# Optimization experiments

Measured on AMD Instinct MI355X. Metric: run time of the kernel, lower is better.

## Reference

```python
import jax, jax.numpy as jnp
import numpy as np

N_NODES = 100000
N_EDGES = 1600000
D_IN, D_HID, D_OUT = 128, 64, 64


def setup_inputs() -> dict:
    key = jax.random.key(0)
    k0, k1, k2, k3 = jax.random.split(key, 4)
    X = jax.random.normal(k0, (N_NODES, D_IN), dtype=jnp.float32)
    E = jax.random.randint(k1, (2, N_EDGES), 0, N_NODES, dtype=jnp.int32)
    W1 = jax.random.normal(k2, (D_IN, D_HID), dtype=jnp.float32) * 0.05
    b1 = jnp.zeros((D_HID,), dtype=jnp.float32)
    W2 = jax.random.normal(k3, (D_HID, D_OUT), dtype=jnp.float32) * 0.05
    b2 = jnp.zeros((D_OUT,), dtype=jnp.float32)
    return {"V": N_NODES, "E": E, "X": X, "W1": W1, "b1": b1, "W2": W2, "b2": b2}


def _gcn_layer(X, W, b, src, dst, norm, n):
    # GCNConv: linear transform (no bias), gather, degree-normalize, scatter-add, + bias
    Xl = X @ W                              # [n, d_out]
    msg = Xl[src] * norm[:, None]           # [n_edges_sl, d_out] gather
    out = jax.ops.segment_sum(msg, dst, num_segments=n)  # scatter-add
    return out + b


def reference(V, E, X, W1, b1, W2, b2):
    n = X.shape[0]
    # add self loops (add_self_loops=True)
    loop = jnp.arange(n, dtype=E.dtype)
    src = jnp.concatenate([E[0], loop])
    dst = jnp.concatenate([E[1], loop])
    # symmetric gcn_norm: deg over target nodes (unit edge weights)
    deg = jax.ops.segment_sum(jnp.ones_like(dst, dtype=X.dtype), dst, num_segments=n)
    dinv = jnp.where(deg > 0, jax.lax.rsqrt(deg), 0.0)
    norm = dinv[src] * dinv[dst]
    H = jax.nn.relu(_gcn_layer(X, W1, b1, src, dst, norm, n))
    # last layer: no ReLU (matches torch module)
    return _gcn_layer(H, W2, b2, src, dst, norm, n)
```

## Files before the change

kernel.cpp:

```cpp
#include <hip/hip_runtime.h>

#define NT 256
#define TILE 256
#define TILE_SH 8
#define BSTRIDE 8192
#define BSTRIDE_SH 13
#define EPB 4096
#define ITB 16
#define NBUCK_PAD 512

static inline int cdiv(long long a, long long b) { return (int)((a + b - 1) / b); }

typedef unsigned int uint32;
typedef unsigned short ushort16;
typedef short bf16x8 __attribute__((ext_vector_type(8)));
typedef float f32x4 __attribute__((ext_vector_type(4)));

__device__ __forceinline__ ushort16 f2bf(float f) {
  uint32 u = __float_as_uint(f);
  u = (u + 0x7FFF + ((u >> 16) & 1)) >> 16;
  return (ushort16)u;
}
__device__ __forceinline__ float bflo(uint32 w) { return __uint_as_float(w << 16); }
__device__ __forceinline__ float bfhi(uint32 w) { return __uint_as_float(w & 0xFFFF0000u); }
__device__ __forceinline__ float bf2f(ushort16 h) { return __uint_as_float(((uint32)h) << 16); }

template <int K>
__device__ __forceinline__ void stage_W(const float* __restrict__ W,
                                        unsigned short* __restrict__ Wt) {
  constexpr int STR = K + 8;
  for (int i = threadIdx.x; i < K * 64; i += NT) {
    int k = i >> 6, nn = i & 63;
    Wt[nn * STR + k] = f2bf(W[i]);
  }
}

template <int K, int BFIN, int SPLIT>
__device__ __forceinline__ void gemm_tile(const void* __restrict__ Xp,
                                          const unsigned short* __restrict__ Wt,
                                          uint2* __restrict__ Yb, int n, int base) {
  constexpr int STR = K + 8;
  const int tid = threadIdx.x;
  const int w = tid >> 6;
  const int lane = tid & 63;
  const int r = lane & 15;
  const int quad = lane >> 4;
  const int rloc = w * 16 + r;
  const int v = base + rloc;

  f32x4 acc[4];
#pragma unroll
  for (int i = 0; i < 4; ++i) acc[i] = (f32x4)(0.f);

  if (BFIN) {
    const uint4* X4 = (const uint4*)Xp;
    bf16x8 xf[K / 32];
#pragma unroll
    for (int ks = 0; ks < K / 32; ++ks) {
      uint4 u = make_uint4(0u, 0u, 0u, 0u);
      if (v < n) u = X4[(size_t)v * (K / 8) + ks * 4 + quad];
      xf[ks] = *(const bf16x8*)&u;
    }
#pragma unroll
    for (int ks = 0; ks < K / 32; ++ks) {
      const int koff = ks * 32 + quad * 8;
#pragma unroll
      for (int nt = 0; nt < 4; ++nt) {
        bf16x8 wf = *(const bf16x8*)&Wt[(nt * 16 + r) * STR + koff];
        acc[nt] = __builtin_amdgcn_mfma_f32_16x16x32_bf16(wf, xf[ks], acc[nt], 0, 0, 0);
      }
    }
  } else {
    const float4* X4 = (const float4*)Xp;
    float4 a[K / 32][2];
#pragma unroll
    for (int ks = 0; ks < K / 32; ++ks) {
      a[ks][0] = make_float4(0.f, 0.f, 0.f, 0.f);
      a[ks][1] = make_float4(0.f, 0.f, 0.f, 0.f);
      if (v < n) {
        a[ks][0] = X4[(size_t)v * (K / 4) + ks * 8 + quad * 2];
        a[ks][1] = X4[(size_t)v * (K / 4) + ks * 8 + quad * 2 + 1];
      }
    }
#pragma unroll
    for (int ks = 0; ks < K / 32; ++ks) {
      float f[8] = {a[ks][0].x, a[ks][0].y, a[ks][0].z, a[ks][0].w,
                    a[ks][1].x, a[ks][1].y, a[ks][1].z, a[ks][1].w};
      bf16x8 xh, xl;
#pragma unroll
      for (int j = 0; j < 8; ++j) {
        ushort16 h = f2bf(f[j]);
        xh[j] = (short)h;
        if (SPLIT) xl[j] = (short)f2bf(f[j] - bf2f(h));
      }
      const int koff = ks * 32 + quad * 8;
#pragma unroll
      for (int nt = 0; nt < 4; ++nt) {
        bf16x8 wf = *(const bf16x8*)&Wt[(nt * 16 + r) * STR + koff];
        if (SPLIT)
          acc[nt] = __builtin_amdgcn_mfma_f32_16x16x32_bf16(wf, xl, acc[nt], 0, 0, 0);
        acc[nt] = __builtin_amdgcn_mfma_f32_16x16x32_bf16(wf, xh, acc[nt], 0, 0, 0);
      }
    }
  }

  if (v < n) {
#pragma unroll
    for (int nt = 0; nt < 4; ++nt) {
      uint2 u;
      u.x = (uint32)f2bf(acc[nt][0]) | ((uint32)f2bf(acc[nt][1]) << 16);
      u.y = (uint32)f2bf(acc[nt][2]) | ((uint32)f2bf(acc[nt][3]) << 16);
      Yb[(size_t)v * 16 + nt * 4 + quad] = u;
    }
  }
}

struct ScatSh {
  int cnt[NBUCK_PAD];
  int lcur[NBUCK_PAD];
  int delta[NBUCK_PAD];
  int hs[NT];
  uint32 sorted[EPB];
  unsigned short bid[EPB];
};
union FusedSh {
  unsigned short wt[64 * 136];
  ScatSh s;
};

__global__ __launch_bounds__(NT, 4) void k_fused(
    const int* __restrict__ src, const int* __restrict__ dst,
    int* __restrict__ bcursor, uint32* __restrict__ buck, int nE, int nbuck,
    int gscat, int ggemm, int ntile, const float* __restrict__ X,
    const float* __restrict__ W1, uint2* __restrict__ Yb, int n) {
  __shared__ FusedSh sm;
  if ((int)blockIdx.x >= gscat) {
    stage_W<128>(W1, sm.wt);
    __syncthreads();
    for (int tile = (int)blockIdx.x - gscat; tile < ntile; tile += ggemm)
      gemm_tile<128, 0, 1>(X, sm.wt, Yb, n, tile * 64);
    return;
  }
  const int t = threadIdx.x;
  for (int i = t; i < NBUCK_PAD; i += NT) sm.s.cnt[i] = 0;
  __syncthreads();
  const int e0 = blockIdx.x * EPB;
  const int ne = min(EPB, nE - e0);
  int dreg[ITB];
#pragma unroll
  for (int it = 0; it < ITB; ++it) {
    int e = e0 + it * NT + t;
    dreg[it] = (e < nE) ? dst[e] : -1;
    if (dreg[it] >= 0) atomicAdd(&sm.s.cnt[dreg[it] >> TILE_SH], 1);
  }
  __syncthreads();
  int c0 = sm.s.cnt[2 * t], c1 = sm.s.cnt[2 * t + 1];
  int ps = c0 + c1;
  sm.s.hs[t] = ps;
  __syncthreads();
  for (int o = 1; o < NT; o <<= 1) {
    int x = (t >= o) ? sm.s.hs[t - o] : 0;
    __syncthreads();
    sm.s.hs[t] += x;
    __syncthreads();
  }
  int lb0 = sm.s.hs[t] - ps;
  int lb1 = lb0 + c0;
  sm.s.lcur[2 * t] = lb0;
  sm.s.lcur[2 * t + 1] = lb1;
  {
    int b0 = 2 * t, b1 = 2 * t + 1;
    if (b0 < nbuck) {
      int g0 = c0 ? atomicAdd(&bcursor[b0], c0) : 0;
      sm.s.delta[b0] = (b0 << BSTRIDE_SH) + g0 - lb0;
    }
    if (b1 < nbuck) {
      int g1 = c1 ? atomicAdd(&bcursor[b1], c1) : 0;
      sm.s.delta[b1] = (b1 << BSTRIDE_SH) + g1 - lb1;
    }
  }
  __syncthreads();
#pragma unroll
  for (int it = 0; it < ITB; ++it) {
    int e = e0 + it * NT + t;
    if (dreg[it] >= 0) {
      int d = dreg[it];
      int b = d >> TILE_SH;
      int p = atomicAdd(&sm.s.lcur[b], 1);
      sm.s.sorted[p] = (uint32)src[e] | ((uint32)(d & (TILE - 1)) << 24);
      sm.s.bid[p] = (unsigned short)b;
    }
  }
  __syncthreads();
  for (int i = t; i < ne; i += NT) {
    int b = sm.s.bid[i];
    int g = sm.s.delta[b] + i;
    if (g < ((b + 1) << BSTRIDE_SH))
      buck[g] = sm.s.sorted[i];
  }
}

__global__ __launch_bounds__(NT) void k_bcsr(const uint32* __restrict__ buck,
                                             const int* __restrict__ bcursor,
                                             int2* __restrict__ rowspan,
                                             float* __restrict__ dinv,
                                             int* __restrict__ srcs, int n) {
  __shared__ int hist[TILE];
  __shared__ int hs[NT];
  __shared__ int off[TILE];
  __shared__ uint32 sarr[BSTRIDE];
  const int b = blockIdx.x;
  const int t = threadIdx.x;
  const int W = b * BSTRIDE;
  const int cntb = min(bcursor[b], BSTRIDE);
  const int v0 = b << TILE_SH;
  const int nv = min(TILE, n - v0);
  hist[t] = 0;
  __syncthreads();
  for (int i = t; i < cntb; i += NT) atomicAdd(&hist[buck[W + i] >> 24], 1);
  __syncthreads();
  int h = hist[t];
  hs[t] = h;
  __syncthreads();
  for (int o = 1; o < NT; o <<= 1) {
    int x = (t >= o) ? hs[t - o] : 0;
    __syncthreads();
    hs[t] += x;
    __syncthreads();
  }
  int ex = hs[t] - h;
  off[t] = ex;
  if (t < nv) {
    rowspan[v0 + t] = make_int2(W + ex, W + ex + h);
    dinv[v0 + t] = rsqrtf((float)(h + 1));
  }
  __syncthreads();
  for (int i = t; i < cntb; i += NT) {
    uint32 w = buck[W + i];
    int ld = (int)(w >> 24);
    int p = atomicAdd(&off[ld], 1);
    sarr[p] = w & 0x00FFFFFFu;
  }
  __syncthreads();
  for (int i = t; i < cntb; i += NT) srcs[W + i] = (int)sarr[i];
}

struct Acc8 {
  float a0, a1, a2, a3, a4, a5, a6, a7;
  __device__ __forceinline__ void madd(uint4 r, float s) {
    a0 = fmaf(bflo(r.x), s, a0); a1 = fmaf(bfhi(r.x), s, a1);
    a2 = fmaf(bflo(r.y), s, a2); a3 = fmaf(bfhi(r.y), s, a3);
    a4 = fmaf(bflo(r.z), s, a4); a5 = fmaf(bfhi(r.z), s, a5);
    a6 = fmaf(bflo(r.w), s, a6); a7 = fmaf(bfhi(r.w), s, a7);
  }
};

template <int RELU, int OUTBF>
__global__ __launch_bounds__(NT) void k_gather(const int2* __restrict__ rowspan,
                                               const int* __restrict__ srcs,
                                               const float* __restrict__ dinv,
                                               const uint4* __restrict__ Xn,
                                               const float* __restrict__ bias,
                                               void* __restrict__ outp, int n) {
  const int gt = blockIdx.x * NT + threadIdx.x;
  const int lane = threadIdx.x & 63;
  const int v = ((gt >> 6) << 1) + (lane >> 5);
  if (v >= n) return;
  const int l5 = lane & 31;
  const int part = l5 & 7;
  const int q = l5 >> 3;
  const int2 rs = rowspan[v];
  const int beg = rs.x, end = rs.y;
  const float dv = dinv[v];
  Acc8 A = {0.f, 0.f, 0.f, 0.f, 0.f, 0.f, 0.f, 0.f};
  int j = beg + q;
  for (; j + 4 < end; j += 8) {
    int s0 = srcs[j];
    int s1 = srcs[j + 4];
    float ds0 = dinv[s0];
    float ds1 = dinv[s1];
    uint4 r0 = Xn[(size_t)s0 * 8 + part];
    uint4 r1 = Xn[(size_t)s1 * 8 + part];
    A.madd(r0, ds0);
    A.madd(r1, ds1);
  }
  if (j < end) {
    int s = srcs[j];
    A.madd(Xn[(size_t)s * 8 + part], dinv[s]);
  }
#pragma unroll
  for (int m = 8; m <= 16; m <<= 1) {
    A.a0 += __shfl_xor(A.a0, m);
    A.a1 += __shfl_xor(A.a1, m);
    A.a2 += __shfl_xor(A.a2, m);
    A.a3 += __shfl_xor(A.a3, m);
    A.a4 += __shfl_xor(A.a4, m);
    A.a5 += __shfl_xor(A.a5, m);
    A.a6 += __shfl_xor(A.a6, m);
    A.a7 += __shfl_xor(A.a7, m);
  }
  if (q == 0) {
    uint4 wv = Xn[(size_t)v * 8 + part];
    const float4* b4 = (const float4*)bias;
    float4 b0 = b4[part * 2], b1 = b4[part * 2 + 1];
    float r0 = dv * (A.a0 + dv * bflo(wv.x)) + b0.x;
    float r1 = dv * (A.a1 + dv * bfhi(wv.x)) + b0.y;
    float r2 = dv * (A.a2 + dv * bflo(wv.y)) + b0.z;
    float r3 = dv * (A.a3 + dv * bfhi(wv.y)) + b0.w;
    float r4 = dv * (A.a4 + dv * bflo(wv.z)) + b1.x;
    float r5 = dv * (A.a5 + dv * bfhi(wv.z)) + b1.y;
    float r6 = dv * (A.a6 + dv * bflo(wv.w)) + b1.z;
    float r7 = dv * (A.a7 + dv * bfhi(wv.w)) + b1.w;
    if (RELU) {
      r0 = fmaxf(r0, 0.f); r1 = fmaxf(r1, 0.f); r2 = fmaxf(r2, 0.f); r3 = fmaxf(r3, 0.f);
      r4 = fmaxf(r4, 0.f); r5 = fmaxf(r5, 0.f); r6 = fmaxf(r6, 0.f); r7 = fmaxf(r7, 0.f);
    }
    if (OUTBF) {
      uint4 u;
      u.x = (uint32)f2bf(r0) | ((uint32)f2bf(r1) << 16);
      u.y = (uint32)f2bf(r2) | ((uint32)f2bf(r3) << 16);
      u.z = (uint32)f2bf(r4) | ((uint32)f2bf(r5) << 16);
      u.w = (uint32)f2bf(r6) | ((uint32)f2bf(r7) << 16);
      ((uint4*)outp)[(size_t)v * 8 + part] = u;
    } else {
      float4* o4 = (float4*)outp;
      o4[(size_t)v * 16 + part * 2] = make_float4(r0, r1, r2, r3);
      o4[(size_t)v * 16 + part * 2 + 1] = make_float4(r4, r5, r6, r7);
    }
  }
}

__global__ __launch_bounds__(NT, 4) void k_gemm2(const void* __restrict__ Xp,
                                                 const float* __restrict__ W,
                                                 uint2* __restrict__ Yb, int n,
                                                 int gg, int ntile) {
  __shared__ unsigned short Wt[64 * 72];
  stage_W<64>(W, Wt);
  __syncthreads();
  for (int tile = (int)blockIdx.x; tile < ntile; tile += gg)
    gemm_tile<64, 1, 0>(Xp, Wt, Yb, n, tile * 64);
}

extern "C" void kernel_launch(void* const* d_in, const int* in_sizes, int n_in,
                              void* d_out, int out_size, void* d_ws, size_t ws_size,
                              hipStream_t stream) {
  const int* E = (const int*)d_in[1];
  const float* X = (const float*)d_in[2];
  const float* W1 = (const float*)d_in[3];
  const float* b1 = (const float*)d_in[4];
  const float* W2 = (const float*)d_in[5];
  const float* b2 = (const float*)d_in[6];
  float* out = (float*)d_out;

  const int n = in_sizes[2] / 128;
  const int nE = in_sizes[1] / 2;
  const int* src = E;
  const int* dst = E + nE;
  const int nbuck = cdiv(n, TILE);

  char* ws = (char*)d_ws;
  size_t off = 0;
  auto alloc = [&](size_t bytes) {
    size_t o = off;
    off = (off + bytes + 255) & ~(size_t)255;
    return (void*)(ws + o);
  };
  int2* rowspan = (int2*)alloc((size_t)n * 8);
  float* dinv = (float*)alloc((size_t)n * 4);
  int* bcursor = (int*)alloc((size_t)nbuck * 4);
  uint32* buck = (uint32*)alloc((size_t)nbuck * BSTRIDE * 4);
  int* srcs = (int*)alloc((size_t)nbuck * BSTRIDE * 4);
  uint2* Xn = (uint2*)alloc((size_t)n * 64 * 2);
  uint2* H = (uint2*)alloc((size_t)n * 64 * 2);

  const int gscat = cdiv(nE, EPB);
  const int ntile = cdiv(n, 64);
  const int ggemm = 1024 - gscat;
  const int gthreads_blocks = cdiv((long long)n * 32, NT);

  hipMemsetAsync(bcursor, 0, (size_t)nbuck * 4, stream);

  k_fused<<<gscat + ggemm, NT, 0, stream>>>(src, dst, bcursor, buck, nE, nbuck,
                                            gscat, ggemm, ntile, X, W1, Xn, n);
  k_bcsr<<<nbuck, NT, 0, stream>>>(buck, bcursor, rowspan, dinv, srcs, n);

  k_gather<1, 1><<<gthreads_blocks, NT, 0, stream>>>(rowspan, srcs, dinv,
                                                     (const uint4*)Xn, b1, H, n);

  k_gemm2<<<1024, NT, 0, stream>>>(H, W2, Xn, n, 1024, ntile);
  k_gather<0, 0><<<gthreads_blocks, NT, 0, stream>>>(rowspan, srcs, dinv,
                                                     (const uint4*)Xn, b2, out, n);
}
```

Baseline: 233.1 us.

## Fuse layer-2 GEMM into layer-1 gather and add dynamic tile scheduling

```diff
diff --git a/kernel.cpp b/kernel.cpp
--- a/kernel.cpp
+++ b/kernel.cpp
@@ -35,7 +35,7 @@
   }
 }
 
-template <int K, int BFIN, int SPLIT>
+template <int K, int SPLIT>
 __device__ __forceinline__ void gemm_tile(const void* __restrict__ Xp,
                                           const unsigned short* __restrict__ Wt,
                                           uint2* __restrict__ Yb, int n, int base) {
@@ -52,55 +52,35 @@
 #pragma unroll
   for (int i = 0; i < 4; ++i) acc[i] = (f32x4)(0.f);
 
-  if (BFIN) {
-    const uint4* X4 = (const uint4*)Xp;
-    bf16x8 xf[K / 32];
-#pragma unroll
-    for (int ks = 0; ks < K / 32; ++ks) {
-      uint4 u = make_uint4(0u, 0u, 0u, 0u);
-      if (v < n) u = X4[(size_t)v * (K / 8) + ks * 4 + quad];
-      xf[ks] = *(const bf16x8*)&u;
-    }
-#pragma unroll
-    for (int ks = 0; ks < K / 32; ++ks) {
-      const int koff = ks * 32 + quad * 8;
-#pragma unroll
-      for (int nt = 0; nt < 4; ++nt) {
-        bf16x8 wf = *(const bf16x8*)&Wt[(nt * 16 + r) * STR + koff];
-        acc[nt] = __builtin_amdgcn_mfma_f32_16x16x32_bf16(wf, xf[ks], acc[nt], 0, 0, 0);
-      }
-    }
-  } else {
-    const float4* X4 = (const float4*)Xp;
-    float4 a[K / 32][2];
-#pragma unroll
-    for (int ks = 0; ks < K / 32; ++ks) {
-      a[ks][0] = make_float4(0.f, 0.f, 0.f, 0.f);
-      a[ks][1] = make_float4(0.f, 0.f, 0.f, 0.f);
-      if (v < n) {
-        a[ks][0] = X4[(size_t)v * (K / 4) + ks * 8 + quad * 2];
-        a[ks][1] = X4[(size_t)v * (K / 4) + ks * 8 + quad * 2 + 1];
-      }
-    }
-#pragma unroll
-    for (int ks = 0; ks < K / 32; ++ks) {
-      float f[8] = {a[ks][0].x, a[ks][0].y, a[ks][0].z, a[ks][0].w,
-                    a[ks][1].x, a[ks][1].y, a[ks][1].z, a[ks][1].w};
-      bf16x8 xh, xl;
-#pragma unroll
-      for (int j = 0; j < 8; ++j) {
-        ushort16 h = f2bf(f[j]);
-        xh[j] = (short)h;
-        if (SPLIT) xl[j] = (short)f2bf(f[j] - bf2f(h));
-      }
-      const int koff = ks * 32 + quad * 8;
-#pragma unroll
-      for (int nt = 0; nt < 4; ++nt) {
-        bf16x8 wf = *(const bf16x8*)&Wt[(nt * 16 + r) * STR + koff];
-        if (SPLIT)
-          acc[nt] = __builtin_amdgcn_mfma_f32_16x16x32_bf16(wf, xl, acc[nt], 0, 0, 0);
-        acc[nt] = __builtin_amdgcn_mfma_f32_16x16x32_bf16(wf, xh, acc[nt], 0, 0, 0);
-      }
+  const float4* X4 = (const float4*)Xp;
+  float4 a[K / 32][2];
+#pragma unroll
+  for (int ks = 0; ks < K / 32; ++ks) {
+    a[ks][0] = make_float4(0.f, 0.f, 0.f, 0.f);
+    a[ks][1] = make_float4(0.f, 0.f, 0.f, 0.f);
+    if (v < n) {
+      a[ks][0] = X4[(size_t)v * (K / 4) + ks * 8 + quad * 2];
+      a[ks][1] = X4[(size_t)v * (K / 4) + ks * 8 + quad * 2 + 1];
+    }
+  }
+#pragma unroll
+  for (int ks = 0; ks < K / 32; ++ks) {
+    float f[8] = {a[ks][0].x, a[ks][0].y, a[ks][0].z, a[ks][0].w,
+                  a[ks][1].x, a[ks][1].y, a[ks][1].z, a[ks][1].w};
+    bf16x8 xh, xl;
+#pragma unroll
+    for (int j = 0; j < 8; ++j) {
+      ushort16 h = f2bf(f[j]);
+      xh[j] = (short)h;
+      if (SPLIT) xl[j] = (short)f2bf(f[j] - bf2f(h));
+    }
+    const int koff = ks * 32 + quad * 8;
+#pragma unroll
+    for (int nt = 0; nt < 4; ++nt) {
+      bf16x8 wf = *(const bf16x8*)&Wt[(nt * 16 + r) * STR + koff];
+      if (SPLIT)
+        acc[nt] = __builtin_amdgcn_mfma_f32_16x16x32_bf16(wf, xl, acc[nt], 0, 0, 0);
+      acc[nt] = __builtin_amdgcn_mfma_f32_16x16x32_bf16(wf, xh, acc[nt], 0, 0, 0);
     }
   }
 
@@ -130,73 +110,81 @@
 
 __global__ __launch_bounds__(NT, 4) void k_fused(
     const int* __restrict__ src, const int* __restrict__ dst,
-    int* __restrict__ bcursor, uint32* __restrict__ buck, int nE, int nbuck,
-    int gscat, int ggemm, int ntile, const float* __restrict__ X,
-    const float* __restrict__ W1, uint2* __restrict__ Yb, int n) {
+    int* __restrict__ bcursor, int* __restrict__ tileCtr,
+    uint32* __restrict__ buck, int nE, int nbuck, int gscat, int ntile,
+    const float* __restrict__ X, const float* __restrict__ W1,
+    uint2* __restrict__ Yb, int n) {
   __shared__ FusedSh sm;
-  if ((int)blockIdx.x >= gscat) {
-    stage_W<128>(W1, sm.wt);
-    __syncthreads();
-    for (int tile = (int)blockIdx.x - gscat; tile < ntile; tile += ggemm)
-      gemm_tile<128, 0, 1>(X, sm.wt, Yb, n, tile * 64);
-    return;
-  }
+  __shared__ int stile;
   const int t = threadIdx.x;
-  for (int i = t; i < NBUCK_PAD; i += NT) sm.s.cnt[i] = 0;
-  __syncthreads();
-  const int e0 = blockIdx.x * EPB;
-  const int ne = min(EPB, nE - e0);
-  int dreg[ITB];
-#pragma unroll
-  for (int it = 0; it < ITB; ++it) {
-    int e = e0 + it * NT + t;
-    dreg[it] = (e < nE) ? dst[e] : -1;
-    if (dreg[it] >= 0) atomicAdd(&sm.s.cnt[dreg[it] >> TILE_SH], 1);
-  }
-  __syncthreads();
-  int c0 = sm.s.cnt[2 * t], c1 = sm.s.cnt[2 * t + 1];
-  int ps = c0 + c1;
-  sm.s.hs[t] = ps;
-  __syncthreads();
-  for (int o = 1; o < NT; o <<= 1) {
-    int x = (t >= o) ? sm.s.hs[t - o] : 0;
-    __syncthreads();
-    sm.s.hs[t] += x;
-    __syncthreads();
-  }
-  int lb0 = sm.s.hs[t] - ps;
-  int lb1 = lb0 + c0;
-  sm.s.lcur[2 * t] = lb0;
-  sm.s.lcur[2 * t + 1] = lb1;
-  {
-    int b0 = 2 * t, b1 = 2 * t + 1;
-    if (b0 < nbuck) {
-      int g0 = c0 ? atomicAdd(&bcursor[b0], c0) : 0;
-      sm.s.delta[b0] = (b0 << BSTRIDE_SH) + g0 - lb0;
-    }
-    if (b1 < nbuck) {
-      int g1 = c1 ? atomicAdd(&bcursor[b1], c1) : 0;
-      sm.s.delta[b1] = (b1 << BSTRIDE_SH) + g1 - lb1;
-    }
-  }
-  __syncthreads();
-#pragma unroll
-  for (int it = 0; it < ITB; ++it) {
-    int e = e0 + it * NT + t;
-    if (dreg[it] >= 0) {
-      int d = dreg[it];
-      int b = d >> TILE_SH;
-      int p = atomicAdd(&sm.s.lcur[b], 1);
-      sm.s.sorted[p] = (uint32)src[e] | ((uint32)(d & (TILE - 1)) << 24);
-      sm.s.bid[p] = (unsigned short)b;
-    }
-  }
-  __syncthreads();
-  for (int i = t; i < ne; i += NT) {
-    int b = sm.s.bid[i];
-    int g = sm.s.delta[b] + i;
-    if (g < ((b + 1) << BSTRIDE_SH))
-      buck[g] = sm.s.sorted[i];
+  if ((int)blockIdx.x < gscat) {
+    for (int i = t; i < NBUCK_PAD; i += NT) sm.s.cnt[i] = 0;
+    __syncthreads();
+    const int e0 = blockIdx.x * EPB;
+    const int ne = min(EPB, nE - e0);
+    int dreg[ITB];
+#pragma unroll
+    for (int it = 0; it < ITB; ++it) {
+      int e = e0 + it * NT + t;
+      dreg[it] = (e < nE) ? dst[e] : -1;
+      if (dreg[it] >= 0) atomicAdd(&sm.s.cnt[dreg[it] >> TILE_SH], 1);
+    }
+    __syncthreads();
+    int c0 = sm.s.cnt[2 * t], c1 = sm.s.cnt[2 * t + 1];
+    int ps = c0 + c1;
+    sm.s.hs[t] = ps;
+    __syncthreads();
+    for (int o = 1; o < NT; o <<= 1) {
+      int x = (t >= o) ? sm.s.hs[t - o] : 0;
+      __syncthreads();
+      sm.s.hs[t] += x;
+      __syncthreads();
+    }
+    int lb0 = sm.s.hs[t] - ps;
+    int lb1 = lb0 + c0;
+    sm.s.lcur[2 * t] = lb0;
+    sm.s.lcur[2 * t + 1] = lb1;
+    {
+      int b0 = 2 * t, b1 = 2 * t + 1;
+      if (b0 < nbuck) {
+        int g0 = c0 ? atomicAdd(&bcursor[b0], c0) : 0;
+        sm.s.delta[b0] = (b0 << BSTRIDE_SH) + g0 - lb0;
+      }
+      if (b1 < nbuck) {
+        int g1 = c1 ? atomicAdd(&bcursor[b1], c1) : 0;
+        sm.s.delta[b1] = (b1 << BSTRIDE_SH) + g1 - lb1;
+      }
+    }
+    __syncthreads();
+#pragma unroll
+    for (int it = 0; it < ITB; ++it) {
+      int e = e0 + it * NT + t;
+      if (dreg[it] >= 0) {
+        int d = dreg[it];
+        int b = d >> TILE_SH;
+        int p = atomicAdd(&sm.s.lcur[b], 1);
+        sm.s.sorted[p] = (uint32)src[e] | ((uint32)(d & (TILE - 1)) << 24);
+        sm.s.bid[p] = (unsigned short)b;
+      }
+    }
+    __syncthreads();
+    for (int i = t; i < ne; i += NT) {
+      int b = sm.s.bid[i];
+      int g = sm.s.delta[b] + i;
+      if (g < ((b + 1) << BSTRIDE_SH))
+        buck[g] = sm.s.sorted[i];
+    }
+    __syncthreads();
+  }
+  stage_W<128>(W1, sm.wt);
+  __syncthreads();
+  for (;;) {
+    if (t == 0) stile = atomicAdd(tileCtr, 1);
+    __syncthreads();
+    int tile = stile;
+    __syncthreads();
+    if (tile >= ntile) break;
+    gemm_tile<128, 1>(X, sm.wt, Yb, n, tile * 64);
   }
 }
 
@@ -255,13 +243,89 @@
   }
 };
 
-template <int RELU, int OUTBF>
-__global__ __launch_bounds__(NT) void k_gather(const int2* __restrict__ rowspan,
-                                               const int* __restrict__ srcs,
-                                               const float* __restrict__ dinv,
-                                               const uint4* __restrict__ Xn,
-                                               const float* __restrict__ bias,
-                                               void* __restrict__ outp, int n) {
+__global__ __launch_bounds__(NT) void k_gather_l1(
+    const int2* __restrict__ rowspan, const int* __restrict__ srcs,
+    const float* __restrict__ dinv, const uint4* __restrict__ Y1,
+    const float* __restrict__ bias, const float* __restrict__ W2,
+    uint32* __restrict__ Y2, int n) {
+  __shared__ float W2s[64 * 64];
+  __shared__ float hrow[8][72];
+  for (int i = threadIdx.x; i < 64 * 64; i += NT) W2s[i] = W2[i];
+
+  const int tid = threadIdx.x;
+  const int lane = tid & 63;
+  const int l5 = lane & 31;
+  const int part = l5 & 7;
+  const int q = l5 >> 3;
+  const int slot = ((tid >> 6) << 1) + (lane >> 5);
+  const int v = blockIdx.x * 8 + slot;
+  const bool act = v < n;
+
+  int2 rs = act ? rowspan[v] : make_int2(0, 0);
+  const int beg = rs.x, end = rs.y;
+  const float dv = act ? dinv[v] : 0.f;
+  Acc8 A = {0.f, 0.f, 0.f, 0.f, 0.f, 0.f, 0.f, 0.f};
+  int j = beg + q;
+  for (; j + 4 < end; j += 8) {
+    int s0 = srcs[j];
+    int s1 = srcs[j + 4];
+    float ds0 = dinv[s0];
+    float ds1 = dinv[s1];
+    uint4 r0 = Y1[(size_t)s0 * 8 + part];
+    uint4 r1 = Y1[(size_t)s1 * 8 + part];
+    A.madd(r0, ds0);
+    A.madd(r1, ds1);
+  }
+  if (j < end) {
+    int s = srcs[j];
+    A.madd(Y1[(size_t)s * 8 + part], dinv[s]);
+  }
+#pragma unroll
+  for (int m = 8; m <= 16; m <<= 1) {
+    A.a0 += __shfl_xor(A.a0, m);
+    A.a1 += __shfl_xor(A.a1, m);
+    A.a2 += __shfl_xor(A.a2, m);
+    A.a3 += __shfl_xor(A.a3, m);
+    A.a4 += __shfl_xor(A.a4, m);
+    A.a5 += __shfl_xor(A.a5, m);
+    A.a6 += __shfl_xor(A.a6, m);
+    A.a7 += __shfl_xor(A.a7, m);
+  }
+  if (q == 0 && act) {
+    uint4 wv = Y1[(size_t)v * 8 + part];
+    const float4* b4 = (const float4*)bias;
+    float4 b0 = b4[part * 2], b1 = b4[part * 2 + 1];
+    float r0 = fmaxf(dv * (A.a0 + dv * bflo(wv.x)) + b0.x, 0.f);
+    float r1 = fmaxf(dv * (A.a1 + dv * bfhi(wv.x)) + b0.y, 0.f);
+    float r2 = fmaxf(dv * (A.a2 + dv * bflo(wv.y)) + b0.z, 0.f);
+    float r3 = fmaxf(dv * (A.a3 + dv * bfhi(wv.y)) + b0.w, 0.f);
+    float r4 = fmaxf(dv * (A.a4 + dv * bflo(wv.z)) + b1.x, 0.f);
+    float r5 = fmaxf(dv * (A.a5 + dv * bfhi(wv.z)) + b1.y, 0.f);
+    float r6 = fmaxf(dv * (A.a6 + dv * bflo(wv.w)) + b1.z, 0.f);
+    float r7 = fmaxf(dv * (A.a7 + dv * bfhi(wv.w)) + b1.w, 0.f);
+    *(float4*)&hrow[slot][part * 8] = make_float4(r0, r1, r2, r3);
+    *(float4*)&hrow[slot][part * 8 + 4] = make_float4(r4, r5, r6, r7);
+  }
+  __syncthreads();
+  float y0 = 0.f, y1 = 0.f;
+#pragma unroll 8
+  for (int k = 0; k < 64; ++k) {
+    float h = hrow[slot][k];
+    y0 = fmaf(h, W2s[k * 64 + 2 * l5], y0);
+    y1 = fmaf(h, W2s[k * 64 + 2 * l5 + 1], y1);
+  }
+  if (act) {
+    uint32 u = (uint32)f2bf(y0) | ((uint32)f2bf(y1) << 16);
+    Y2[(size_t)v * 32 + l5] = u;
+  }
+}
+
+__global__ __launch_bounds__(NT) void k_gather2(const int2* __restrict__ rowspan,
+                                                const int* __restrict__ srcs,
+                                                const float* __restrict__ dinv,
+                                                const uint4* __restrict__ Xn,
+                                                const float* __restrict__ bias,
+                                                float* __restrict__ outp, int n) {
   const int gt = blockIdx.x * NT + threadIdx.x;
   const int lane = threadIdx.x & 63;
   const int v = ((gt >> 6) << 1) + (lane >> 5);
@@ -311,34 +375,10 @@
     float r5 = dv * (A.a5 + dv * bfhi(wv.z)) + b1.y;
     float r6 = dv * (A.a6 + dv * bflo(wv.w)) + b1.z;
     float r7 = dv * (A.a7 + dv * bfhi(wv.w)) + b1.w;
-    if (RELU) {
-      r0 = fmaxf(r0, 0.f); r1 = fmaxf(r1, 0.f); r2 = fmaxf(r2, 0.f); r3 = fmaxf(r3, 0.f);
-      r4 = fmaxf(r4, 0.f); r5 = fmaxf(r5, 0.f); r6 = fmaxf(r6, 0.f); r7 = fmaxf(r7, 0.f);
-    }
-    if (OUTBF) {
-      uint4 u;
-      u.x = (uint32)f2bf(r0) | ((uint32)f2bf(r1) << 16);
-      u.y = (uint32)f2bf(r2) | ((uint32)f2bf(r3) << 16);
-      u.z = (uint32)f2bf(r4) | ((uint32)f2bf(r5) << 16);
-      u.w = (uint32)f2bf(r6) | ((uint32)f2bf(r7) << 16);
-      ((uint4*)outp)[(size_t)v * 8 + part] = u;
-    } else {
-      float4* o4 = (float4*)outp;
-      o4[(size_t)v * 16 + part * 2] = make_float4(r0, r1, r2, r3);
-      o4[(size_t)v * 16 + part * 2 + 1] = make_float4(r4, r5, r6, r7);
-    }
-  }
-}
-
-__global__ __launch_bounds__(NT, 4) void k_gemm2(const void* __restrict__ Xp,
-                                                 const float* __restrict__ W,
-                                                 uint2* __restrict__ Yb, int n,
-                                                 int gg, int ntile) {
-  __shared__ unsigned short Wt[64 * 72];
-  stage_W<64>(W, Wt);
-  __syncthreads();
-  for (int tile = (int)blockIdx.x; tile < ntile; tile += gg)
-    gemm_tile<64, 1, 0>(Xp, Wt, Yb, n, tile * 64);
+    float4* o4 = (float4*)outp;
+    o4[(size_t)v * 16 + part * 2] = make_float4(r0, r1, r2, r3);
+    o4[(size_t)v * 16 + part * 2 + 1] = make_float4(r4, r5, r6, r7);
+  }
 }
 
 extern "C" void kernel_launch(void* const* d_in, const int* in_sizes, int n_in,
@@ -367,27 +407,28 @@
   };
   int2* rowspan = (int2*)alloc((size_t)n * 8);
   float* dinv = (float*)alloc((size_t)n * 4);
-  int* bcursor = (int*)alloc((size_t)nbuck * 4);
+  int* bcursor = (int*)alloc((size_t)(nbuck + 1) * 4);
+  int* tileCtr = bcursor + nbuck;
   uint32* buck = (uint32*)alloc((size_t)nbuck * BSTRIDE * 4);
   int* srcs = (int*)alloc((size_t)nbuck * BSTRIDE * 4);
-  uint2* Xn = (uint2*)alloc((size_t)n * 64 * 2);
-  uint2* H = (uint2*)alloc((size_t)n * 64 * 2);
+  uint2* Y1 = (uint2*)alloc((size_t)n * 64 * 2);
+  uint2* Y2 = (uint2*)alloc((size_t)n * 64 * 2);
 
   const int gscat = cdiv(nE, EPB);
   const int ntile = cdiv(n, 64);
-  const int ggemm = 1024 - gscat;
+  const int gfused = 1024;
   const int gthreads_blocks = cdiv((long long)n * 32, NT);
 
-  hipMemsetAsync(bcursor, 0, (size_t)nbuck * 4, stream);
-
-  k_fused<<<gscat + ggemm, NT, 0, stream>>>(src, dst, bcursor, buck, nE, nbuck,
-                                            gscat, ggemm, ntile, X, W1, Xn, n);
+  hipMemsetAsync(bcursor, 0, (size_t)(nbuck + 1) * 4, stream);
+
+  k_fused<<<gfused, NT, 0, stream>>>(src, dst, bcursor, tileCtr, buck, nE,
+                                     nbuck, gscat, ntile, X, W1, Y1, n);
   k_bcsr<<<nbuck, NT, 0, stream>>>(buck, bcursor, rowspan, dinv, srcs, n);
 
-  k_gather<1, 1><<<gthreads_blocks, NT, 0, stream>>>(rowspan, srcs, dinv,
-                                                     (const uint4*)Xn, b1, H, n);
-
-  k_gemm2<<<1024, NT, 0, stream>>>(H, W2, Xn, n, 1024, ntile);
-  k_gather<0, 0><<<gthreads_blocks, NT, 0, stream>>>(rowspan, srcs, dinv,
-                                                     (const uint4*)Xn, b2, out, n);
-}
+  k_gather_l1<<<gthreads_blocks, NT, 0, stream>>>(rowspan, srcs, dinv,
+                                                  (const uint4*)Y1, b1, W2,
+                                                  (uint32*)Y2, n);
+
+  k_gather2<<<gthreads_blocks, NT, 0, stream>>>(rowspan, srcs, dinv,
+                                                (const uint4*)Y2, b2, out, n);
+}
```

Measured after the change: 261.3 us. 12.1% more time.
